# Kernel optimization log

Measured on AMD Instinct MI355X. Metric: run time of the kernel, lower is better.

## Reference

```python
import jax, jax.numpy as jnp
import numpy as np

N_NODES = 50000   # n_nodes
N_EDGES = 400000  # n_edges = N_NODES * avg_degree(8)
H = 32            # n_hidden
N_ETYPES = 8      # len(edge_type)
N_LAYER = 3


def setup_inputs() -> dict:
    key = jax.random.key(0)
    ks = jax.random.split(key, 12)
    feature = jax.random.normal(ks[0], (N_NODES, H), dtype=jnp.float32)
    src = jax.random.randint(ks[1], (N_EDGES,), 0, N_NODES, dtype=jnp.int32)
    dst = jax.random.randint(ks[2], (N_EDGES,), 0, N_NODES, dtype=jnp.int32)
    param_id = jax.random.randint(ks[3], (N_EDGES,), 0, N_ETYPES, dtype=jnp.int32)
    # nn.Parameter(...).normal_(): std-1 gaussian per-edge-type weight matrices
    param = jax.random.normal(ks[4], (N_ETYPES, H, H), dtype=jnp.float32)
    # final MLP([H, 2H, 2H, 1]) params (jax convention: weight is (in, out))
    def lin(k, fan_in, fan_out):
        kw, kb = jax.random.split(k)
        bound = 1.0 / np.sqrt(fan_in)
        w = jax.random.uniform(kw, (fan_in, fan_out), jnp.float32, -bound, bound)
        b = jax.random.uniform(kb, (fan_out,), jnp.float32, -bound, bound)
        return w, b
    w1, b1 = lin(ks[5], H, 2 * H)
    w2, b2 = lin(ks[6], 2 * H, 2 * H)
    w3, b3 = lin(ks[7], 2 * H, 1)
    return {"feature": feature, "param": param,
            "w1": w1, "b1": b1, "w2": w2, "b2": b2, "w3": w3, "b3": b3,
            "src": src, "dst": dst, "param_id": param_id}


def reference(feature, param, w1, b1, w2, b2, w3, b3, src, dst, param_id):
    # Edge weights assigned once before the layer loop (as in GNN.forward)
    W = param[param_id]                                  # (E, H, H)
    out = feature                                        # (N, H)
    for _ in range(N_LAYER):
        # message: gather src feats + per-edge matmul ('ei,eij->ej')
        msg = jnp.einsum('ei,eij->ej', out[src], W)      # (E, H)
        # reduce: sum messages into destination nodes
        agg = jax.ops.segment_sum(msg, dst, num_segments=N_NODES)  # (N, H)
        # WeightedConv final output (its internal MLP result is discarded)
        out = (out + agg) * 0.5
    # F.normalize(dim=-1), eps=1e-12
    nrm = jnp.linalg.norm(out, axis=-1, keepdims=True)
    x = out / jnp.maximum(nrm, 1e-12)
    # MLP([H, 2H, 2H, 1]): Linear, Tanh, Linear, Tanh, Linear
    h = jnp.tanh(x @ w1 + b1)
    h = jnp.tanh(h @ w2 + b2)
    logits = (h @ w3 + b3)[..., 0]                       # (N,)
    return jax.nn.sigmoid(logits)
```

## Files before the change

kernel.cpp:

```cpp
#include <hip/hip_runtime.h>
#include <math.h>

#define N_NODES 50000
#define N_EDGES 400000
#define HD 32
#define N_ET 8
#define CAP 64

__device__ inline void fma4(float4& a, float s, const float4 w) {
    a.x = fmaf(s, w.x, a.x);
    a.y = fmaf(s, w.y, a.y);
    a.z = fmaf(s, w.z, a.z);
    a.w = fmaf(s, w.w, a.w);
}
__device__ inline void add4(float4& a, const float4 v) {
    a.x += v.x; a.y += v.y; a.z += v.z; a.w += v.w;
}

__global__ __launch_bounds__(256) void k_count(
    const int* __restrict__ src, const int* __restrict__ dst,
    const int* __restrict__ pid, int* __restrict__ deg,
    int* __restrict__ payload)
{
    int e = blockIdx.x * blockDim.x + threadIdx.x;
    if (e >= N_EDGES) return;
    int d = dst[e];
    int pos = atomicAdd(&deg[d], 1);
    if (pos < CAP) payload[d * CAP + pos] = pid[e] * N_NODES + src[e];
}

__global__ __launch_bounds__(256) void k_transform(
    const float* __restrict__ xin, const float* __restrict__ param,
    float* __restrict__ Y)
{
    int n = blockIdx.x * blockDim.x + threadIdx.x;
    if (n >= N_NODES) return;
    const int t = blockIdx.y;
    const size_t base = (size_t)n * HD;
    const float* W = param + t * (HD * HD);

    float x[HD];
    #pragma unroll
    for (int q = 0; q < 8; ++q) {
        float4 v = *(const float4*)(xin + base + q * 4);
        x[q * 4 + 0] = v.x; x[q * 4 + 1] = v.y;
        x[q * 4 + 2] = v.z; x[q * 4 + 3] = v.w;
    }

    float4 acc[8];
    #pragma unroll
    for (int q = 0; q < 8; ++q) acc[q] = make_float4(0.f, 0.f, 0.f, 0.f);
    #pragma unroll
    for (int i = 0; i < HD; ++i) {
        float xi = x[i];
        #pragma unroll
        for (int q = 0; q < 8; ++q)
            fma4(acc[q], xi, *(const float4*)(W + i * HD + q * 4));
    }
    float* yo = Y + (size_t)t * N_NODES * HD + base;
    #pragma unroll
    for (int q = 0; q < 8; ++q) *(float4*)(yo + q * 4) = acc[q];
}

__global__ __launch_bounds__(256) void k_gather(
    const int* __restrict__ deg, const int* __restrict__ payload,
    const float* __restrict__ Y, const float* __restrict__ xin,
    float* __restrict__ xout)
{
    int tid = blockIdx.x * blockDim.x + threadIdx.x;
    int node = tid >> 3, sl = tid & 7;
    if (node >= N_NODES) return;
    int d = deg[node];
    if (d > CAP) d = CAP;
    const int* pl = payload + node * CAP;

    float4 a0 = make_float4(0.f,0.f,0.f,0.f), a1 = a0, a2 = a0, a3 = a0;
    int k = 0;
    for (; k + 4 <= d; k += 4) {
        int4 c = *(const int4*)(pl + k);
        float4 v0 = *(const float4*)(Y + (size_t)c.x * HD + sl * 4);
        float4 v1 = *(const float4*)(Y + (size_t)c.y * HD + sl * 4);
        float4 v2 = *(const float4*)(Y + (size_t)c.z * HD + sl * 4);
        float4 v3 = *(const float4*)(Y + (size_t)c.w * HD + sl * 4);
        add4(a0, v0); add4(a1, v1); add4(a2, v2); add4(a3, v3);
    }
    for (; k < d; ++k) {
        int c = pl[k];
        add4(a0, *(const float4*)(Y + (size_t)c * HD + sl * 4));
    }
    add4(a0, a1); add4(a2, a3); add4(a0, a2);

    const size_t off = (size_t)node * HD + sl * 4;
    float4 x = *(const float4*)(xin + off);
    x.x = (x.x + a0.x) * 0.5f;
    x.y = (x.y + a0.y) * 0.5f;
    x.z = (x.z + a0.z) * 0.5f;
    x.w = (x.w + a0.w) * 0.5f;
    *(float4*)(xout + off) = x;
}

__global__ __launch_bounds__(256) void k_final(
    const float* __restrict__ cur,
    const float* __restrict__ w1, const float* __restrict__ b1,
    const float* __restrict__ w2, const float* __restrict__ b2,
    const float* __restrict__ w3, const float* __restrict__ b3,
    float* __restrict__ out)
{
    int gt = blockIdx.x * blockDim.x + threadIdx.x;
    int node = gt >> 3, q = gt & 7;
    if (node >= N_NODES) return;

    float4 xo = *(const float4*)(cur + (size_t)node * HD + q * 4);
    float ss = xo.x * xo.x + xo.y * xo.y + xo.z * xo.z + xo.w * xo.w;
    ss += __shfl_xor(ss, 1, 8);
    ss += __shfl_xor(ss, 2, 8);
    ss += __shfl_xor(ss, 4, 8);
    float rn = 1.0f / fmaxf(sqrtf(ss), 1e-12f);
    xo.x *= rn; xo.y *= rn; xo.z *= rn; xo.w *= rn;

    float4 h0 = *(const float4*)(b1 + q * 8);
    float4 h1 = *(const float4*)(b1 + q * 8 + 4);
    for (int s = 0; s < 8; ++s) {
        float m0 = __shfl(xo.x, s, 8);
        float m1 = __shfl(xo.y, s, 8);
        float m2 = __shfl(xo.z, s, 8);
        float m3 = __shfl(xo.w, s, 8);
        const float* wr = w1 + (s * 4) * 64 + q * 8;
        fma4(h0, m0, *(const float4*)(wr));
        fma4(h1, m0, *(const float4*)(wr + 4));
        fma4(h0, m1, *(const float4*)(wr + 64));
        fma4(h1, m1, *(const float4*)(wr + 68));
        fma4(h0, m2, *(const float4*)(wr + 128));
        fma4(h1, m2, *(const float4*)(wr + 132));
        fma4(h0, m3, *(const float4*)(wr + 192));
        fma4(h1, m3, *(const float4*)(wr + 196));
    }
    float t1[8];
    t1[0] = tanhf(h0.x); t1[1] = tanhf(h0.y); t1[2] = tanhf(h0.z); t1[3] = tanhf(h0.w);
    t1[4] = tanhf(h1.x); t1[5] = tanhf(h1.y); t1[6] = tanhf(h1.z); t1[7] = tanhf(h1.w);

    float4 g0 = *(const float4*)(b2 + q * 8);
    float4 g1 = *(const float4*)(b2 + q * 8 + 4);
    for (int s = 0; s < 8; ++s) {
        const float* wr = w2 + (s * 8) * 64 + q * 8;
        #pragma unroll
        for (int c = 0; c < 8; ++c) {
            float m = __shfl(t1[c], s, 8);
            fma4(g0, m, *(const float4*)(wr + c * 64));
            fma4(g1, m, *(const float4*)(wr + c * 64 + 4));
        }
    }

    float4 wa = *(const float4*)(w3 + q * 8);
    float4 wb = *(const float4*)(w3 + q * 8 + 4);
    float p = 0.f;
    p = fmaf(tanhf(g0.x), wa.x, p);
    p = fmaf(tanhf(g0.y), wa.y, p);
    p = fmaf(tanhf(g0.z), wa.z, p);
    p = fmaf(tanhf(g0.w), wa.w, p);
    p = fmaf(tanhf(g1.x), wb.x, p);
    p = fmaf(tanhf(g1.y), wb.y, p);
    p = fmaf(tanhf(g1.z), wb.z, p);
    p = fmaf(tanhf(g1.w), wb.w, p);
    p += __shfl_xor(p, 1, 8);
    p += __shfl_xor(p, 2, 8);
    p += __shfl_xor(p, 4, 8);
    if (q == 0) out[node] = 1.0f / (1.0f + expf(-(p + b3[0])));
}

extern "C" void kernel_launch(void* const* d_in, const int* in_sizes, int n_in,
                              void* d_out, int out_size, void* d_ws, size_t ws_size,
                              hipStream_t stream) {
    const float* feature = (const float*)d_in[0];
    const float* param   = (const float*)d_in[1];
    const float* w1      = (const float*)d_in[2];
    const float* b1      = (const float*)d_in[3];
    const float* w2      = (const float*)d_in[4];
    const float* b2      = (const float*)d_in[5];
    const float* w3      = (const float*)d_in[6];
    const float* b3      = (const float*)d_in[7];
    const int*   src     = (const int*)d_in[8];
    const int*   dst     = (const int*)d_in[9];
    const int*   pid     = (const int*)d_in[10];
    float* out = (float*)d_out;

    const size_t Y_BYTES   = (size_t)N_ET * N_NODES * HD * sizeof(float);
    const size_t NH_BYTES  = (size_t)N_NODES * HD * sizeof(float);
    const size_t DEG_BYTES = (size_t)N_NODES * sizeof(int);
    char* p = (char*)d_ws;
    float* Y       = (float*)p;            p += Y_BYTES;
    float* cur     = (float*)p;            p += NH_BYTES;
    int*   deg     = (int*)p;              p += DEG_BYTES;
    int*   payload = (int*)p;

    const int TB = 256;
    const int gT = (N_NODES + TB - 1) / TB;
    const int gE = (N_EDGES + TB - 1) / TB;
    const int gG = (N_NODES * 8 + TB - 1) / TB;
    dim3 gridT(gT, N_ET);

    hipMemsetAsync(deg, 0, DEG_BYTES, stream);
    k_count<<<gE, TB, 0, stream>>>(src, dst, pid, deg, payload);

    k_transform<<<gridT, TB, 0, stream>>>(feature, param, Y);
    k_gather<<<gG, TB, 0, stream>>>(deg, payload, Y, feature, cur);
    k_transform<<<gridT, TB, 0, stream>>>(cur, param, Y);
    k_gather<<<gG, TB, 0, stream>>>(deg, payload, Y, cur, cur);
    k_transform<<<gridT, TB, 0, stream>>>(cur, param, Y);
    k_gather<<<gG, TB, 0, stream>>>(deg, payload, Y, cur, cur);
    k_final<<<gG, TB, 0, stream>>>(cur, w1, b1, w2, b2, w3, b3, out);
}
```

Measured before the change: 266.3 us.

## Bin edges by (dst, type), aggregate before transform, fuse layers with final MLP

Edges are bucketed per destination node and edge type, so each node sums raw source features per type and then applies that type's 32x32 weight once, instead of precomputing 8 transformed copies of every node. This drops the large per-layer transform kernel and its 8xNxH intermediate buffer, and the last layer is fused into the normalize+MLP kernel. The cost is a per-node loop over 8 types with shuffles and weight reads, plus a 16-entry cap per (node, type) bin that silently drops edges beyond it. It also ping-pongs between two buffers rather than updating in place.

```diff
diff --git a/kernel.cpp b/kernel.cpp
--- a/kernel.cpp
+++ b/kernel.cpp
@@ -5,7 +5,7 @@
 #define N_EDGES 400000
 #define HD 32
 #define N_ET 8
-#define CAP 64
+#define CAP_T 16
 
 __device__ inline void fma4(float4& a, float s, const float4 w) {
     a.x = fmaf(s, w.x, a.x);
@@ -19,98 +19,92 @@
 
 __global__ __launch_bounds__(256) void k_count(
     const int* __restrict__ src, const int* __restrict__ dst,
-    const int* __restrict__ pid, int* __restrict__ deg,
+    const int* __restrict__ pid, int* __restrict__ cnt,
     int* __restrict__ payload)
 {
     int e = blockIdx.x * blockDim.x + threadIdx.x;
     if (e >= N_EDGES) return;
-    int d = dst[e];
-    int pos = atomicAdd(&deg[d], 1);
-    if (pos < CAP) payload[d * CAP + pos] = pid[e] * N_NODES + src[e];
-}
-
-__global__ __launch_bounds__(256) void k_transform(
+    int bin = dst[e] * N_ET + pid[e];
+    int pos = atomicAdd(&cnt[bin], 1);
+    if (pos < CAP_T) payload[(size_t)bin * CAP_T + pos] = src[e];
+}
+
+__device__ __forceinline__ float4 layer_combine(
+    int node, int q, const int* __restrict__ cnt, const int* __restrict__ payload,
+    const float* __restrict__ x, const float* __restrict__ param)
+{
+    float4 out = make_float4(0.f, 0.f, 0.f, 0.f);
+    for (int t = 0; t < N_ET; ++t) {
+        int c = cnt[node * N_ET + t];
+        if (c > CAP_T) c = CAP_T;
+        if (c == 0) continue;
+        const int* pl = payload + ((size_t)node * N_ET + t) * CAP_T;
+        float4 s = make_float4(0.f, 0.f, 0.f, 0.f);
+        int k = 0;
+        for (; k + 4 <= c; k += 4) {
+            int4 e4 = *(const int4*)(pl + k);
+            float4 v0 = *(const float4*)(x + (size_t)e4.x * HD + q * 4);
+            float4 v1 = *(const float4*)(x + (size_t)e4.y * HD + q * 4);
+            float4 v2 = *(const float4*)(x + (size_t)e4.z * HD + q * 4);
+            float4 v3 = *(const float4*)(x + (size_t)e4.w * HD + q * 4);
+            add4(s, v0); add4(s, v1); add4(s, v2); add4(s, v3);
+        }
+        for (; k < c; ++k)
+            add4(s, *(const float4*)(x + (size_t)pl[k] * HD + q * 4));
+
+        const float* W = param + t * (HD * HD);
+        #pragma unroll
+        for (int sl = 0; sl < 8; ++sl) {
+            float m0 = __shfl(s.x, sl, 8);
+            float m1 = __shfl(s.y, sl, 8);
+            float m2 = __shfl(s.z, sl, 8);
+            float m3 = __shfl(s.w, sl, 8);
+            const float* wr = W + (sl * 4) * HD + q * 4;
+            fma4(out, m0, *(const float4*)(wr));
+            fma4(out, m1, *(const float4*)(wr + HD));
+            fma4(out, m2, *(const float4*)(wr + 2 * HD));
+            fma4(out, m3, *(const float4*)(wr + 3 * HD));
+        }
+    }
+    return out;
+}
+
+__global__ __launch_bounds__(256) void k_layer(
+    const int* __restrict__ cnt, const int* __restrict__ payload,
     const float* __restrict__ xin, const float* __restrict__ param,
-    float* __restrict__ Y)
-{
-    int n = blockIdx.x * blockDim.x + threadIdx.x;
-    if (n >= N_NODES) return;
-    const int t = blockIdx.y;
-    const size_t base = (size_t)n * HD;
-    const float* W = param + t * (HD * HD);
-
-    float x[HD];
-    #pragma unroll
-    for (int q = 0; q < 8; ++q) {
-        float4 v = *(const float4*)(xin + base + q * 4);
-        x[q * 4 + 0] = v.x; x[q * 4 + 1] = v.y;
-        x[q * 4 + 2] = v.z; x[q * 4 + 3] = v.w;
-    }
-
-    float4 acc[8];
-    #pragma unroll
-    for (int q = 0; q < 8; ++q) acc[q] = make_float4(0.f, 0.f, 0.f, 0.f);
-    #pragma unroll
-    for (int i = 0; i < HD; ++i) {
-        float xi = x[i];
-        #pragma unroll
-        for (int q = 0; q < 8; ++q)
-            fma4(acc[q], xi, *(const float4*)(W + i * HD + q * 4));
-    }
-    float* yo = Y + (size_t)t * N_NODES * HD + base;
-    #pragma unroll
-    for (int q = 0; q < 8; ++q) *(float4*)(yo + q * 4) = acc[q];
-}
-
-__global__ __launch_bounds__(256) void k_gather(
-    const int* __restrict__ deg, const int* __restrict__ payload,
-    const float* __restrict__ Y, const float* __restrict__ xin,
     float* __restrict__ xout)
 {
     int tid = blockIdx.x * blockDim.x + threadIdx.x;
-    int node = tid >> 3, sl = tid & 7;
+    int node = tid >> 3, q = tid & 7;
     if (node >= N_NODES) return;
-    int d = deg[node];
-    if (d > CAP) d = CAP;
-    const int* pl = payload + node * CAP;
-
-    float4 a0 = make_float4(0.f,0.f,0.f,0.f), a1 = a0, a2 = a0, a3 = a0;
-    int k = 0;
-    for (; k + 4 <= d; k += 4) {
-        int4 c = *(const int4*)(pl + k);
-        float4 v0 = *(const float4*)(Y + (size_t)c.x * HD + sl * 4);
-        float4 v1 = *(const float4*)(Y + (size_t)c.y * HD + sl * 4);
-        float4 v2 = *(const float4*)(Y + (size_t)c.z * HD + sl * 4);
-        float4 v3 = *(const float4*)(Y + (size_t)c.w * HD + sl * 4);
-        add4(a0, v0); add4(a1, v1); add4(a2, v2); add4(a3, v3);
-    }
-    for (; k < d; ++k) {
-        int c = pl[k];
-        add4(a0, *(const float4*)(Y + (size_t)c * HD + sl * 4));
-    }
-    add4(a0, a1); add4(a2, a3); add4(a0, a2);
-
-    const size_t off = (size_t)node * HD + sl * 4;
-    float4 x = *(const float4*)(xin + off);
-    x.x = (x.x + a0.x) * 0.5f;
-    x.y = (x.y + a0.y) * 0.5f;
-    x.z = (x.z + a0.z) * 0.5f;
-    x.w = (x.w + a0.w) * 0.5f;
-    *(float4*)(xout + off) = x;
-}
-
-__global__ __launch_bounds__(256) void k_final(
-    const float* __restrict__ cur,
+    float4 agg = layer_combine(node, q, cnt, payload, xin, param);
+    const size_t off = (size_t)node * HD + q * 4;
+    float4 xo = *(const float4*)(xin + off);
+    xo.x = (xo.x + agg.x) * 0.5f;
+    xo.y = (xo.y + agg.y) * 0.5f;
+    xo.z = (xo.z + agg.z) * 0.5f;
+    xo.w = (xo.w + agg.w) * 0.5f;
+    *(float4*)(xout + off) = xo;
+}
+
+__global__ __launch_bounds__(256) void k_layer_final(
+    const int* __restrict__ cnt, const int* __restrict__ payload,
+    const float* __restrict__ xin, const float* __restrict__ param,
     const float* __restrict__ w1, const float* __restrict__ b1,
     const float* __restrict__ w2, const float* __restrict__ b2,
     const float* __restrict__ w3, const float* __restrict__ b3,
     float* __restrict__ out)
 {
-    int gt = blockIdx.x * blockDim.x + threadIdx.x;
-    int node = gt >> 3, q = gt & 7;
+    int tid = blockIdx.x * blockDim.x + threadIdx.x;
+    int node = tid >> 3, q = tid & 7;
     if (node >= N_NODES) return;
-
-    float4 xo = *(const float4*)(cur + (size_t)node * HD + q * 4);
+    float4 agg = layer_combine(node, q, cnt, payload, xin, param);
+    float4 xo = *(const float4*)(xin + (size_t)node * HD + q * 4);
+    xo.x = (xo.x + agg.x) * 0.5f;
+    xo.y = (xo.y + agg.y) * 0.5f;
+    xo.z = (xo.z + agg.z) * 0.5f;
+    xo.w = (xo.w + agg.w) * 0.5f;
+
     float ss = xo.x * xo.x + xo.y * xo.y + xo.z * xo.z + xo.w * xo.w;
     ss += __shfl_xor(ss, 1, 8);
     ss += __shfl_xor(ss, 2, 8);
@@ -184,29 +178,24 @@
     const int*   pid     = (const int*)d_in[10];
     float* out = (float*)d_out;
 
-    const size_t Y_BYTES   = (size_t)N_ET * N_NODES * HD * sizeof(float);
+    const size_t CNT_BYTES = (size_t)N_NODES * N_ET * sizeof(int);
+    const size_t PAY_BYTES = (size_t)N_NODES * N_ET * CAP_T * sizeof(int);
     const size_t NH_BYTES  = (size_t)N_NODES * HD * sizeof(float);
-    const size_t DEG_BYTES = (size_t)N_NODES * sizeof(int);
     char* p = (char*)d_ws;
-    float* Y       = (float*)p;            p += Y_BYTES;
-    float* cur     = (float*)p;            p += NH_BYTES;
-    int*   deg     = (int*)p;              p += DEG_BYTES;
-    int*   payload = (int*)p;
+    int*   cnt     = (int*)p;              p += CNT_BYTES;
+    int*   payload = (int*)p;              p += PAY_BYTES;
+    float* c0      = (float*)p;            p += NH_BYTES;
+    float* c1      = (float*)p;
 
     const int TB = 256;
-    const int gT = (N_NODES + TB - 1) / TB;
     const int gE = (N_EDGES + TB - 1) / TB;
-    const int gG = (N_NODES * 8 + TB - 1) / TB;
-    dim3 gridT(gT, N_ET);
-
-    hipMemsetAsync(deg, 0, DEG_BYTES, stream);
-    k_count<<<gE, TB, 0, stream>>>(src, dst, pid, deg, payload);
-
-    k_transform<<<gridT, TB, 0, stream>>>(feature, param, Y);
-    k_gather<<<gG, TB, 0, stream>>>(deg, payload, Y, feature, cur);
-    k_transform<<<gridT, TB, 0, stream>>>(cur, param, Y);
-    k_gather<<<gG, TB, 0, stream>>>(deg, payload, Y, cur, cur);
-    k_transform<<<gridT, TB, 0, stream>>>(cur, param, Y);
-    k_gather<<<gG, TB, 0, stream>>>(deg, payload, Y, cur, cur);
-    k_final<<<gG, TB, 0, stream>>>(cur, w1, b1, w2, b2, w3, b3, out);
-}
+    const int gL = (N_NODES * 8 + TB - 1) / TB;
+
+    hipMemsetAsync(cnt, 0, CNT_BYTES, stream);
+    k_count<<<gE, TB, 0, stream>>>(src, dst, pid, cnt, payload);
+
+    k_layer<<<gL, TB, 0, stream>>>(cnt, payload, feature, param, c0);
+    k_layer<<<gL, TB, 0, stream>>>(cnt, payload, c0, param, c1);
+    k_layer_final<<<gL, TB, 0, stream>>>(cnt, payload, c1, param,
+                                         w1, b1, w2, b2, w3, b3, out);
+}
```

Measured after the change: 400.0 us. +50.2%, slower.
